# Optimization experiments

Hardware: AMD Instinct MI355X
Metric: run time of the kernel (lower is better)

## Reference

```python
import jax, jax.numpy as jnp
import numpy as np

B, T, D = 2, 2048, 1024
H, DH = 16, 64  # heads, head_dim; inner_dim = H*DH = D
EPS = 1e-6


def _rmsnorm(x, g):
    # torch.nn.RMSNorm over last dim with affine weight g
    return x * jax.lax.rsqrt(jnp.mean(x * x, axis=-1, keepdims=True) + EPS) * g


def _interleaved_rope(x, cos, sin):
    # x: [B, T, D]; pairs (x0, x1) rotated: rot = [-x1, x0, -x3, x2, ...]
    b, t, d = x.shape
    x2 = x.reshape(b, t, d // 2, 2)
    rot = jnp.stack([-x2[..., 1], x2[..., 0]], axis=-1).reshape(b, t, d)
    return x * cos + rot * sin


def setup_inputs() -> dict:
    key = jax.random.key(0)
    ks = jax.random.split(key, 8)
    hidden_states = jax.random.normal(ks[0], (B, T, D), dtype=jnp.float32)
    cos = jax.random.uniform(ks[1], (1, T, D), dtype=jnp.float32)
    sin = jax.random.uniform(ks[2], (1, T, D), dtype=jnp.float32)
    s = 0.02  # init scale for weights
    wq = jax.random.normal(ks[3], (D, D), dtype=jnp.float32) * s
    wk = jax.random.normal(ks[4], (D, D), dtype=jnp.float32) * s
    wv = jax.random.normal(ks[5], (D, D), dtype=jnp.float32) * s
    wo = jax.random.normal(ks[6], (D, D), dtype=jnp.float32) * s
    bq = jnp.zeros((D,), jnp.float32)
    bk = jnp.zeros((D,), jnp.float32)
    bv = jnp.zeros((D,), jnp.float32)
    bo = jnp.zeros((D,), jnp.float32)
    gq = jnp.ones((D,), jnp.float32)
    gk = jnp.ones((D,), jnp.float32)
    return {
        'hidden_states': hidden_states, 'cos': cos, 'sin': sin,
        'wq': wq, 'bq': bq, 'wk': wk, 'bk': bk, 'wv': wv, 'bv': bv,
        'gq': gq, 'gk': gk, 'wo': wo, 'bo': bo,
    }


def reference(hidden_states, cos, sin, wq, bq, wk, bk, wv, bv, gq, gk, wo, bo):
    # QKV projections (weights stored as [in, out]) + RMSNorm(q,k) + RoPE
    q = _interleaved_rope(_rmsnorm(hidden_states @ wq + bq, gq), cos, sin)
    k = _interleaved_rope(_rmsnorm(hidden_states @ wk + bk, gk), cos, sin)
    v = hidden_states @ wv + bv

    # split heads: [B, T, D] -> [B, H, T, DH]
    def split(x):
        return x.reshape(B, T, H, DH).transpose(0, 2, 1, 3)
    q, k, v = split(q), split(k), split(v)

    scale = 1.0 / jnp.sqrt(jnp.float32(DH))
    scores = jnp.einsum('bhqd,bhkd->bhqk', q, k) * scale
    attn = jax.nn.softmax(scores, axis=-1)
    out = jnp.einsum('bhqk,bhkd->bhqd', attn, v)

    # merge heads + output projection
    out = out.transpose(0, 2, 1, 3).reshape(B, T, D)
    return out @ wo + bo
```

## Files before the change

### kernel.cpp

```cpp
#include <hip/hip_runtime.h>

typedef _Float16 f16;
typedef _Float16 f16x8 __attribute__((ext_vector_type(8)));
typedef _Float16 f16x4 __attribute__((ext_vector_type(4)));
typedef _Float16 f16x2 __attribute__((ext_vector_type(2)));
typedef float f32x4 __attribute__((ext_vector_type(4)));

#define MFMA(a, b, c) __builtin_amdgcn_mfma_f32_16x16x32_f16(a, b, c, 0, 0, 0)
#define PKRTZ(a, b) __builtin_bit_cast(f16x2, __builtin_amdgcn_cvt_pkrtz(a, b))

__device__ __forceinline__ void gload16(const void* g, void* l) {
  __builtin_amdgcn_global_load_lds((const __attribute__((address_space(1))) char*)g,
                                   (__attribute__((address_space(3))) char*)l, 16, 0, 0);
}


__global__ __launch_bounds__(256) void k_cvt_hidden(const float* __restrict__ x, f16* __restrict__ y) {
  int i = blockIdx.x * 256 + threadIdx.x;
  float4 v = ((const float4*)x)[i];
  f16x4 h; h[0] = (f16)v.x; h[1] = (f16)v.y; h[2] = (f16)v.z; h[3] = (f16)v.w;
  ((f16x4*)y)[i] = h;
}

__global__ __launch_bounds__(256) void k_cvt_w(const float* __restrict__ w0, const float* __restrict__ w1,
                                               const float* __restrict__ w2, const float* __restrict__ w3,
                                               f16* __restrict__ wt) {
  int z = blockIdx.z;
  const float* w = z == 0 ? w0 : z == 1 ? w1 : z == 2 ? w2 : w3;
  f16* dst = wt + (size_t)z * 1024 * 1024;
  __shared__ float tile[64][65];
  int t = threadIdx.x;
  int k0 = blockIdx.x * 64, n0 = blockIdx.y * 64;
  int cr = t >> 4, cc = (t & 15) * 4;
#pragma unroll
  for (int p = 0; p < 4; p++) {
    int r = cr + p * 16;
    float4 v = *(const float4*)&w[(size_t)(k0 + r) * 1024 + n0 + cc];
    tile[r][cc + 0] = v.x; tile[r][cc + 1] = v.y; tile[r][cc + 2] = v.z; tile[r][cc + 3] = v.w;
  }
  __syncthreads();
#pragma unroll
  for (int p = 0; p < 4; p++) {
    int nn = cr + p * 16;
    f16x4 h;
    h[0] = (f16)tile[cc + 0][nn]; h[1] = (f16)tile[cc + 1][nn];
    h[2] = (f16)tile[cc + 2][nn]; h[3] = (f16)tile[cc + 3][nn];
    *(f16x4*)&dst[(size_t)(n0 + nn) * 1024 + k0 + cc] = h;
  }
}

template <bool OUTF32>
__device__ __forceinline__ void gemm_core(const f16* __restrict__ A, const f16* __restrict__ W,
                                          const float* __restrict__ bias,
                                          f16* __restrict__ oh, float* __restrict__ of) {
  __shared__ f16 Al[128 * 64];
  __shared__ f16 Bl[128 * 64];
  const int t = threadIdx.x;
  const int lane = t & 63, wid = t >> 6;
  const int lr = lane & 15, lg = lane >> 4;
  const int m0 = blockIdx.x * 128, n0 = blockIdx.y * 128;
  const int wm = wid >> 1, wn = wid & 1;
  const int lrow = lane >> 3;
  const int cb = (((lane & 7) ^ lrow) << 4);

  f32x4 acc[4][4] = {};

  for (int k0 = 0; k0 < 1024; k0 += 64) {
    __syncthreads();
#pragma unroll
    for (int it = 0; it < 4; it++) {
      int rbase = it * 32 + wid * 8;
      int row = rbase + lrow;
      gload16((const char*)&A[(size_t)(m0 + row) * 1024 + k0] + cb, (char*)Al + rbase * 128);
      gload16((const char*)&W[(size_t)(n0 + row) * 1024 + k0] + cb, (char*)Bl + rbase * 128);
    }
    __syncthreads();
    f16x8 af[2][4], bf[2][4];
#pragma unroll
    for (int x = 0; x < 4; x++) {
      int ra = wm * 64 + x * 16 + lr;
      int rb = wn * 64 + x * 16 + lr;
#pragma unroll
      for (int kh = 0; kh < 2; kh++) {
        int ca = (kh * 64 + lg * 16) ^ ((lr & 7) << 4);
        af[kh][x] = *(const f16x8*)((char*)Al + ra * 128 + ca);
        bf[kh][x] = *(const f16x8*)((char*)Bl + rb * 128 + ca);
      }
    }
#pragma unroll
    for (int kh = 0; kh < 2; kh++)
#pragma unroll
      for (int mt = 0; mt < 4; mt++)
#pragma unroll
        for (int nt = 0; nt < 4; nt++)
          acc[mt][nt] = MFMA(af[kh][mt], bf[kh][nt], acc[mt][nt]);
  }
#pragma unroll
  for (int mt = 0; mt < 4; mt++) {
#pragma unroll
    for (int nt = 0; nt < 4; nt++) {
      int col = n0 + wn * 64 + nt * 16 + lr;
      float bcol = bias[col];
#pragma unroll
      for (int e = 0; e < 4; e++) {
        int row = m0 + wm * 64 + mt * 16 + lg * 4 + e;
        float val = acc[mt][nt][e] + bcol;
        if (OUTF32) of[(size_t)row * 1024 + col] = val;
        else        oh[(size_t)row * 1024 + col] = (f16)val;
      }
    }
  }
}

__global__ __launch_bounds__(256, 2) void k_gemm_qkv(const f16* __restrict__ A, const f16* __restrict__ wt,
                                                     const float* __restrict__ bq, const float* __restrict__ bk,
                                                     const float* __restrict__ bv,
                                                     f16* __restrict__ q, f16* __restrict__ k, f16* __restrict__ v) {
  int z = blockIdx.z;
  gemm_core<false>(A, wt + (size_t)z * 1024 * 1024,
                   z == 0 ? bq : z == 1 ? bk : bv,
                   z == 0 ? q : z == 1 ? k : v, nullptr);
}

__global__ __launch_bounds__(256, 2) void k_gemm_o(const f16* __restrict__ A, const f16* __restrict__ wt,
                                                   const float* __restrict__ bo, float* __restrict__ out) {
  gemm_core<true>(A, wt, bo, nullptr, out);
}

__global__ __launch_bounds__(256) void k_normrope(f16* __restrict__ qh, f16* __restrict__ kh,
                                                  const float* __restrict__ gq, const float* __restrict__ gk,
                                                  const float* __restrict__ cs, const float* __restrict__ sn) {
  int row = blockIdx.x, which = blockIdx.y;
  f16* buf = which ? kh : qh;
  const float* g = which ? gk : gq;
  int t = threadIdx.x, c4 = t * 4;
  f16x4 xv = *(const f16x4*)&buf[(size_t)row * 1024 + c4];
  float x0 = xv[0], x1 = xv[1], x2 = xv[2], x3 = xv[3];
  float ss = x0 * x0 + x1 * x1 + x2 * x2 + x3 * x3;
#pragma unroll
  for (int off = 1; off < 64; off <<= 1) ss += __shfl_xor(ss, off);
  __shared__ float red[4];
  if ((t & 63) == 0) red[t >> 6] = ss;
  __syncthreads();
  float inv = rsqrtf((red[0] + red[1] + red[2] + red[3]) * (1.0f / 1024.0f) + 1e-6f);
  int tt = row & 2047;
  float4 cv = *(const float4*)&cs[(size_t)tt * 1024 + c4];
  float4 sv = *(const float4*)&sn[(size_t)tt * 1024 + c4];
  float4 gv = *(const float4*)&g[c4];
  float y0 = x0 * inv * gv.x, y1 = x1 * inv * gv.y, y2 = x2 * inv * gv.z, y3 = x3 * inv * gv.w;
  f16x4 ov;
  ov[0] = (f16)(y0 * cv.x - y1 * sv.x);
  ov[1] = (f16)(y1 * cv.y + y0 * sv.y);
  ov[2] = (f16)(y2 * cv.z - y3 * sv.z);
  ov[3] = (f16)(y3 * cv.w + y2 * sv.w);
  *(f16x4*)&buf[(size_t)row * 1024 + c4] = ov;
}

__global__ __launch_bounds__(256) void k_vtrans(const f16* __restrict__ vh, f16* __restrict__ vt) {
  __shared__ f16 tile[64][65];
  int t = threadIdx.x;
  int t0 = blockIdx.x * 64;
  int bh = blockIdx.y;
  int b = bh >> 4, h = bh & 15;
  int rr = t >> 3, c8 = (t & 7) * 8;
#pragma unroll
  for (int p = 0; p < 2; p++) {
    int r = p * 32 + rr;
    f16x8 v = *(const f16x8*)&vh[(size_t)(b * 2048 + t0 + r) * 1024 + h * 64 + c8];
#pragma unroll
    for (int j = 0; j < 8; j++) tile[r][c8 + j] = v[j];
  }
  __syncthreads();
#pragma unroll
  for (int p = 0; p < 2; p++) {
    int dh = p * 32 + rr;
    f16x8 o;
#pragma unroll
    for (int j = 0; j < 8; j++) o[j] = tile[c8 + j][dh];
    *(f16x8*)&vt[((size_t)bh * 64 + dh) * 2048 + t0 + c8] = o;
  }
}

#define ASWZ(row) ((((row) & 3) | (((row) & 8) >> 1)) << 4)

__global__ __launch_bounds__(256, 4) void k_attn(const f16* __restrict__ qh, const f16* __restrict__ kh,
                                                 const f16* __restrict__ vt, f16* __restrict__ ao) {
  __shared__ f16 Kl[64 * 64];
  __shared__ f16 Vl[64 * 64];
  const int t = threadIdx.x;
  const int lane = t & 63, wid = t >> 6;
  const int lr = lane & 15, lg = lane >> 4;
  const int lgb = lg << 4;
  const int b = blockIdx.y >> 4, h = blockIdx.y & 15;
  const int q0 = blockIdx.x * 64 + wid * 16;
  const f16* Qb = qh + ((size_t)(b * 2048 + q0)) * 1024 + h * 64;
  f16x8 qf0 = *(const f16x8*)&Qb[(size_t)lr * 1024 + lg * 8];
  f16x8 qf1 = *(const f16x8*)&Qb[(size_t)lr * 1024 + 32 + lg * 8];
  const f16* Kg = kh + ((size_t)b * 2048) * 1024 + h * 64;
  const f16* Vg = vt + ((size_t)blockIdx.y) * 64 * 2048;
  const int lrow = lane >> 3;
  const int sg = (lane & 7) << 4;
  const float sc = 0.125f * 1.44269504088896340736f;
  float m = -1e30f, l = 0.f;
  f32x4 acc[4] = {};

  for (int kv0 = 0; kv0 < 2048; kv0 += 64) {
    __syncthreads();
#pragma unroll
    for (int i = 0; i < 2; i++) {
      int rbase = (i * 4 + wid) * 8;
      int row = rbase + lrow;
      int cswz = sg ^ ASWZ(row);
      gload16((const char*)(Kg + (size_t)(kv0 + row) * 1024) + cswz, (char*)Kl + rbase * 128);
      gload16((const char*)(Vg + (size_t)row * 2048 + kv0) + cswz, (char*)Vl + rbase * 128);
    }
    __syncthreads();

    f32x4 s[4];
#pragma unroll
    for (int ks = 0; ks < 4; ks++) {
      int key = ((lr >> 2) << 3) + (lr & 3) + ((ks & 1) << 2) + ((ks >> 1) << 5);
      int sw = ASWZ(key);
      f16x8 kf0 = *(const f16x8*)((char*)Kl + key * 128 + (lgb ^ sw));
      f16x8 kf1 = *(const f16x8*)((char*)Kl + key * 128 + ((64 + lgb) ^ sw));
      f32x4 z = {};
      z = MFMA(kf0, qf0, z);
      z = MFMA(kf1, qf1, z);
      s[ks] = z;
    }

    float smax = -1e30f;
#pragma unroll
    for (int ks = 0; ks < 4; ks++)
#pragma unroll
      for (int e = 0; e < 4; e++) smax = fmaxf(smax, s[ks][e]);
    smax = fmaxf(smax, __shfl_xor(smax, 16));
    smax = fmaxf(smax, __shfl_xor(smax, 32));
    float mn = fmaxf(m, smax * sc);
    float al = exp2f(m - mn);
    m = mn;
    float sum = 0.f;
    union { f16x8 v; f16x2 h[4]; } u[2];
#pragma unroll
    for (int ks = 0; ks < 4; ks++) {
      float p0 = exp2f(fmaf(s[ks][0], sc, -mn));
      float p1 = exp2f(fmaf(s[ks][1], sc, -mn));
      float p2 = exp2f(fmaf(s[ks][2], sc, -mn));
      float p3 = exp2f(fmaf(s[ks][3], sc, -mn));
      sum += (p0 + p1) + (p2 + p3);
      u[ks >> 1].h[(ks & 1) * 2 + 0] = PKRTZ(p0, p1);
      u[ks >> 1].h[(ks & 1) * 2 + 1] = PKRTZ(p2, p3);
    }
    sum += __shfl_xor(sum, 16);
    sum += __shfl_xor(sum, 32);
    l = l * al + sum;
    float alq[4];
#pragma unroll
    for (int e = 0; e < 4; e++) alq[e] = __shfl(al, lg * 4 + e);
#pragma unroll
    for (int ds = 0; ds < 4; ds++)
#pragma unroll
      for (int e = 0; e < 4; e++) acc[ds][e] *= alq[e];

#pragma unroll
    for (int ds = 0; ds < 4; ds++) {
      int vrow = ds * 16 + lr;
      int sw = ASWZ(vrow);
      f16x8 vf0 = *(const f16x8*)((char*)Vl + vrow * 128 + (lgb ^ sw));
      f16x8 vf1 = *(const f16x8*)((char*)Vl + vrow * 128 + ((64 + lgb) ^ sw));
      acc[ds] = MFMA(u[0].v, vf0, acc[ds]);
      acc[ds] = MFMA(u[1].v, vf1, acc[ds]);
    }
  }

  float lf[4];
#pragma unroll
  for (int e = 0; e < 4; e++) lf[e] = 1.f / __shfl(l, lg * 4 + e);
#pragma unroll
  for (int e = 0; e < 4; e++) {
    size_t row = (size_t)(b * 2048 + q0 + lg * 4 + e);
#pragma unroll
    for (int ds = 0; ds < 4; ds++)
      ao[row * 1024 + h * 64 + ds * 16 + lr] = (f16)(acc[ds][e] * lf[e]);
  }
}

extern "C" void kernel_launch(void* const* d_in, const int* in_sizes, int n_in,
                              void* d_out, int out_size, void* d_ws, size_t ws_size,
                              hipStream_t stream) {
  const float* hid  = (const float*)d_in[0];
  const float* cosb = (const float*)d_in[1];
  const float* sinb = (const float*)d_in[2];
  const float* wq = (const float*)d_in[3];
  const float* bq = (const float*)d_in[4];
  const float* wk = (const float*)d_in[5];
  const float* bk = (const float*)d_in[6];
  const float* wv = (const float*)d_in[7];
  const float* bv = (const float*)d_in[8];
  const float* gq = (const float*)d_in[9];
  const float* gk = (const float*)d_in[10];
  const float* wo = (const float*)d_in[11];
  const float* bo = (const float*)d_in[12];
  float* out = (float*)d_out;

  char* ws = (char*)d_ws;
  f16* aH  = (f16*)(ws);
  f16* wt  = (f16*)(ws + ((size_t)8 << 20));
  f16* qh  = (f16*)(ws + ((size_t)16 << 20));
  f16* khb = (f16*)(ws + ((size_t)24 << 20));
  f16* vhb = (f16*)(ws + ((size_t)32 << 20));
  f16* vtb = (f16*)(ws + ((size_t)40 << 20));
  f16* ao  = (f16*)(ws + ((size_t)48 << 20));

  k_cvt_hidden<<<dim3(4096), dim3(256), 0, stream>>>(hid, aH);
  k_cvt_w<<<dim3(16, 16, 4), dim3(256), 0, stream>>>(wq, wk, wv, wo, wt);
  k_gemm_qkv<<<dim3(32, 8, 3), dim3(256), 0, stream>>>(aH, wt, bq, bk, bv, qh, khb, vhb);
  k_normrope<<<dim3(4096, 2), dim3(256), 0, stream>>>(qh, khb, gq, gk, cosb, sinb);
  k_vtrans<<<dim3(32, 32), dim3(256), 0, stream>>>(vhb, vtb);
  k_attn<<<dim3(32, 32), dim3(256), 0, stream>>>(qh, khb, vtb, ao);
  k_gemm_o<<<dim3(32, 8, 1), dim3(256), 0, stream>>>(ao, wt + (size_t)3 * 1024 * 1024, bo, out);
}
```

Before: 162.4 us.

## Double-buffer K/V tiles, lazy softmax rescale, and remap blocks for L2 locality

The attention kernel now stages K/V into two LDS buffers, prefetching the next tile while computing on the current one, and drops one barrier per iteration. Online-softmax rescaling is skipped unless the running max grows by more than a threshold (8 in log2 units), which saves exp and multiply work on most tiles. Block indices are remapped so that neighbouring blocks share head/batch groups, and the max reduction is flattened. This doubles LDS use, which may lower occupancy. The lazy rescale lets probabilities reach up to 2^8 before being cast to fp16, which adds some precision and overflow risk.

```diff
diff --git a/kernel.cpp b/kernel.cpp
--- a/kernel.cpp
+++ b/kernel.cpp
@@ -185,92 +185,115 @@
 
 __global__ __launch_bounds__(256, 4) void k_attn(const f16* __restrict__ qh, const f16* __restrict__ kh,
                                                  const f16* __restrict__ vt, f16* __restrict__ ao) {
-  __shared__ f16 Kl[64 * 64];
-  __shared__ f16 Vl[64 * 64];
+  __shared__ f16 Kl[2][64 * 64];
+  __shared__ f16 Vl[2][64 * 64];
   const int t = threadIdx.x;
   const int lane = t & 63, wid = t >> 6;
   const int lr = lane & 15, lg = lane >> 4;
   const int lgb = lg << 4;
-  const int b = blockIdx.y >> 4, h = blockIdx.y & 15;
-  const int q0 = blockIdx.x * 64 + wid * 16;
+  const int raw = blockIdx.y * 32 + blockIdx.x;
+  const int mybh = ((raw & 7) << 2) | ((raw >> 3) & 3);
+  const int myq = raw >> 5;
+  const int b = mybh >> 4, h = mybh & 15;
+  const int q0 = myq * 64 + wid * 16;
   const f16* Qb = qh + ((size_t)(b * 2048 + q0)) * 1024 + h * 64;
   f16x8 qf0 = *(const f16x8*)&Qb[(size_t)lr * 1024 + lg * 8];
   f16x8 qf1 = *(const f16x8*)&Qb[(size_t)lr * 1024 + 32 + lg * 8];
   const f16* Kg = kh + ((size_t)b * 2048) * 1024 + h * 64;
-  const f16* Vg = vt + ((size_t)blockIdx.y) * 64 * 2048;
+  const f16* Vg = vt + ((size_t)mybh) * 64 * 2048;
   const int lrow = lane >> 3;
   const int sg = (lane & 7) << 4;
   const float sc = 0.125f * 1.44269504088896340736f;
   float m = -1e30f, l = 0.f;
   f32x4 acc[4] = {};
 
-  for (int kv0 = 0; kv0 < 2048; kv0 += 64) {
-    __syncthreads();
+  auto stage = [&](int kvo, int bs) {
 #pragma unroll
     for (int i = 0; i < 2; i++) {
       int rbase = (i * 4 + wid) * 8;
       int row = rbase + lrow;
       int cswz = sg ^ ASWZ(row);
-      gload16((const char*)(Kg + (size_t)(kv0 + row) * 1024) + cswz, (char*)Kl + rbase * 128);
-      gload16((const char*)(Vg + (size_t)row * 2048 + kv0) + cswz, (char*)Vl + rbase * 128);
-    }
-    __syncthreads();
+      gload16((const char*)(Kg + (size_t)(kvo + row) * 1024) + cswz, (char*)&Kl[bs][0] + rbase * 128);
+      gload16((const char*)(Vg + (size_t)row * 2048 + kvo) + cswz, (char*)&Vl[bs][0] + rbase * 128);
+    }
+  };
+
+  stage(0, 0);
+  __syncthreads();
+  int cur = 0;
+
+  for (int kv0 = 0; kv0 < 2048; kv0 += 64) {
+    if (kv0 + 64 < 2048) stage(kv0 + 64, cur ^ 1);
+    const char* Kb = (const char*)&Kl[cur][0];
+    const char* Vb = (const char*)&Vl[cur][0];
 
     f32x4 s[4];
 #pragma unroll
     for (int ks = 0; ks < 4; ks++) {
       int key = ((lr >> 2) << 3) + (lr & 3) + ((ks & 1) << 2) + ((ks >> 1) << 5);
       int sw = ASWZ(key);
-      f16x8 kf0 = *(const f16x8*)((char*)Kl + key * 128 + (lgb ^ sw));
-      f16x8 kf1 = *(const f16x8*)((char*)Kl + key * 128 + ((64 + lgb) ^ sw));
+      f16x8 kf0 = *(const f16x8*)(Kb + key * 128 + (lgb ^ sw));
+      f16x8 kf1 = *(const f16x8*)(Kb + key * 128 + ((64 + lgb) ^ sw));
       f32x4 z = {};
       z = MFMA(kf0, qf0, z);
       z = MFMA(kf1, qf1, z);
       s[ks] = z;
     }
 
-    float smax = -1e30f;
-#pragma unroll
-    for (int ks = 0; ks < 4; ks++)
-#pragma unroll
-      for (int e = 0; e < 4; e++) smax = fmaxf(smax, s[ks][e]);
+    float smax = fmaxf(fmaxf(s[0][0], s[0][1]), s[0][2]);
+    smax = fmaxf(fmaxf(smax, s[0][3]), s[1][0]);
+    smax = fmaxf(fmaxf(smax, s[1][1]), s[1][2]);
+    smax = fmaxf(fmaxf(smax, s[1][3]), s[2][0]);
+    smax = fmaxf(fmaxf(smax, s[2][1]), s[2][2]);
+    smax = fmaxf(fmaxf(smax, s[2][3]), s[3][0]);
+    smax = fmaxf(fmaxf(smax, s[3][1]), s[3][2]);
+    smax = fmaxf(smax, s[3][3]);
     smax = fmaxf(smax, __shfl_xor(smax, 16));
     smax = fmaxf(smax, __shfl_xor(smax, 32));
-    float mn = fmaxf(m, smax * sc);
-    float al = exp2f(m - mn);
-    m = mn;
+    float smc = smax * sc;
+
+    if (!__all(smc - m <= 8.f)) {
+      float mn = fmaxf(m, smc);
+      float al = exp2f(m - mn);
+      m = mn;
+      float alq[4];
+#pragma unroll
+      for (int e = 0; e < 4; e++) alq[e] = __shfl(al, lg * 4 + e);
+      l *= al;
+#pragma unroll
+      for (int ds = 0; ds < 4; ds++)
+#pragma unroll
+        for (int e = 0; e < 4; e++) acc[ds][e] *= alq[e];
+    }
+
     float sum = 0.f;
     union { f16x8 v; f16x2 h[4]; } u[2];
 #pragma unroll
     for (int ks = 0; ks < 4; ks++) {
-      float p0 = exp2f(fmaf(s[ks][0], sc, -mn));
-      float p1 = exp2f(fmaf(s[ks][1], sc, -mn));
-      float p2 = exp2f(fmaf(s[ks][2], sc, -mn));
-      float p3 = exp2f(fmaf(s[ks][3], sc, -mn));
+      float p0 = exp2f(fmaf(s[ks][0], sc, -m));
+      float p1 = exp2f(fmaf(s[ks][1], sc, -m));
+      float p2 = exp2f(fmaf(s[ks][2], sc, -m));
+      float p3 = exp2f(fmaf(s[ks][3], sc, -m));
       sum += (p0 + p1) + (p2 + p3);
       u[ks >> 1].h[(ks & 1) * 2 + 0] = PKRTZ(p0, p1);
       u[ks >> 1].h[(ks & 1) * 2 + 1] = PKRTZ(p2, p3);
     }
     sum += __shfl_xor(sum, 16);
     sum += __shfl_xor(sum, 32);
-    l = l * al + sum;
-    float alq[4];
-#pragma unroll
-    for (int e = 0; e < 4; e++) alq[e] = __shfl(al, lg * 4 + e);
-#pragma unroll
-    for (int ds = 0; ds < 4; ds++)
-#pragma unroll
-      for (int e = 0; e < 4; e++) acc[ds][e] *= alq[e];
+    l += sum;
 
 #pragma unroll
     for (int ds = 0; ds < 4; ds++) {
       int vrow = ds * 16 + lr;
       int sw = ASWZ(vrow);
-      f16x8 vf0 = *(const f16x8*)((char*)Vl + vrow * 128 + (lgb ^ sw));
-      f16x8 vf1 = *(const f16x8*)((char*)Vl + vrow * 128 + ((64 + lgb) ^ sw));
+      f16x8 vf0 = *(const f16x8*)(Vb + vrow * 128 + (lgb ^ sw));
+      f16x8 vf1 = *(const f16x8*)(Vb + vrow * 128 + ((64 + lgb) ^ sw));
       acc[ds] = MFMA(u[0].v, vf0, acc[ds]);
       acc[ds] = MFMA(u[1].v, vf1, acc[ds]);
     }
+
+    __syncthreads();
+    cur ^= 1;
   }
 
   float lf[4];
```

Measured after the change: 154.9 us. 4.6% less time.
